# Kernel tuning notes

Hardware: AMD Instinct MI355X
Metric: run time of the kernel (lower is better)

## Reference

```python
import jax, jax.numpy as jnp
import numpy as np

DIM = 2048
N_HEADS = 16
HEAD_DIM = DIM // N_HEADS
GROUP_SIZE = 128
THRESHOLD = 0.5
EPS = 1e-8
B, T = 2, 2048


def _ternary_dequant(w):
    # groupwise absmean ternary quantize + dequant; DIM % GROUP_SIZE == 0 so no pad
    O, I = w.shape
    g = I // GROUP_SIZE
    wg = w.reshape(O, g, GROUP_SIZE)
    scale = jnp.clip(jnp.mean(jnp.abs(wg), axis=-1, keepdims=True), EPS)
    wn = wg / scale
    q = jnp.where(wn > THRESHOLD, 1.0, jnp.where(wn < -THRESHOLD, -1.0, 0.0))
    return (q * scale).reshape(O, I)


def _bitlinear(x, w):
    # STE: forward uses quantized weight
    w_ste = w + jax.lax.stop_gradient(_ternary_dequant(w) - w)
    return x @ w_ste.T


def _rope_tables(t, head_dim, base=10000.0):
    half = head_dim // 2
    inv_freq = 1.0 / (base ** (jnp.arange(half, dtype=jnp.float32) / half))
    freqs = jnp.outer(jnp.arange(t, dtype=jnp.float32), inv_freq)  # [T, half]
    return jnp.cos(freqs), jnp.sin(freqs)


def _apply_rope(x, cos, sin):
    # x: [B, H, T, D]
    d = x.shape[-1]
    x1, x2 = x[..., : d // 2], x[..., d // 2 :]
    cos = cos[None, None, :, :]
    sin = sin[None, None, :, :]
    return jnp.concatenate([x1 * cos - x2 * sin, x1 * sin + x2 * cos], axis=-1)


def setup_inputs() -> dict:
    key = jax.random.key(0)
    ks = jax.random.split(key, 5)
    std = 1.0 / np.sqrt(DIM)
    return {
        "x": jax.random.normal(ks[0], (B, T, DIM), dtype=jnp.float32),
        "w_q": jax.random.normal(ks[1], (DIM, DIM), dtype=jnp.float32) * std,
        "w_k": jax.random.normal(ks[2], (DIM, DIM), dtype=jnp.float32) * std,
        "w_v": jax.random.normal(ks[3], (DIM, DIM), dtype=jnp.float32) * std,
        "w_o": jax.random.normal(ks[4], (DIM, DIM), dtype=jnp.float32) * std,
    }


def reference(x, w_q, w_k, w_v, w_o):
    b, t, c = x.shape
    scale = HEAD_DIM ** -0.5

    def split_heads(y):
        return y.reshape(b, t, N_HEADS, HEAD_DIM).transpose(0, 2, 1, 3)  # [B,H,T,D]

    q = split_heads(_bitlinear(x, w_q))
    k = split_heads(_bitlinear(x, w_k))
    v = split_heads(_bitlinear(x, w_v))

    cos, sin = _rope_tables(t, HEAD_DIM)
    q = _apply_rope(q, cos, sin)
    k = _apply_rope(k, cos, sin)

    scores = jnp.einsum("bhqd,bhkd->bhqk", q, k) * scale
    causal = jnp.triu(jnp.ones((t, t), dtype=bool), k=1)
    scores = jnp.where(causal[None, None], -jnp.inf, scores)
    probs = jax.nn.softmax(scores, axis=-1)
    y = jnp.einsum("bhqk,bhkd->bhqd", probs, v)
    y = y.transpose(0, 2, 1, 3).reshape(b, t, c)
    return _bitlinear(y, w_o)
```

## Files before the change

### kernel.cpp

```cpp
#include <hip/hip_runtime.h>
#include <stdint.h>
#include <math.h>

#define DIMC 2048
#define NHEADS 16
#define HDIM 128
#define TSEQ 2048
#define NTOK 4096

using bf16x8 = __attribute__((ext_vector_type(8))) short;
using f32x4  = __attribute__((ext_vector_type(4))) float;

typedef __attribute__((address_space(1))) const void gas_void;
typedef __attribute__((address_space(3))) void las_void;

static __device__ __forceinline__ unsigned short f2b(float f) {
  union { float f; unsigned int u; } a; a.f = f;
  unsigned int u = a.u;
  u = (u + 0x7fffu + ((u >> 16) & 1u)) >> 16;
  return (unsigned short)u;
}
static __device__ __forceinline__ float b2f(unsigned short s) {
  union { unsigned int u; float f; } a; a.u = ((unsigned int)s) << 16;
  return a.f;
}

__global__ void detect_dtype(const unsigned short* __restrict__ xs,
                             int* __restrict__ flag)
{
  const int lane = threadIdx.x;
  const unsigned short u = xs[2 * lane];
  const int e = (u >> 7) & 0xFF;
  const bool plausible = (e >= 112) && (e <= 135);
  const unsigned long long m = __ballot(plausible);
  if (lane == 0) *flag = (__popcll(m) >= 32) ? 1 : 0;
}

static __device__ __forceinline__ void dequant_one(
    const void* __restrict__ w, unsigned short* __restrict__ o,
    int grp, int lane, int isbf16)
{
  float a, bq;
  if (isbf16) {
    const unsigned int pk =
        ((const unsigned int*)((const unsigned short*)w + (long)grp * 128))[lane];
    a  = b2f((unsigned short)(pk & 0xffffu));
    bq = b2f((unsigned short)(pk >> 16));
  } else {
    const float2 v = ((const float2*)((const float*)w + (long)grp * 128))[lane];
    a = v.x; bq = v.y;
  }
  double s = fabs((double)a) + fabs((double)bq);
  #pragma unroll
  for (int off = 1; off < 64; off <<= 1) s += __shfl_xor(s, off);
  double scale = s * (1.0 / 128.0);
  if (scale < 1e-8) scale = 1e-8;
  const float fs = (float)scale;
  const double wn0 = (double)a / scale;
  const double wn1 = (double)bq / scale;
  const float q0 = (wn0 > 0.5) ? fs : ((wn0 < -0.5) ? -fs : 0.0f);
  const float q1 = (wn1 > 0.5) ? fs : ((wn1 < -0.5) ? -fs : 0.0f);
  const unsigned int opk = (unsigned int)f2b(q0) | ((unsigned int)f2b(q1) << 16);
  ((unsigned int*)o)[(long)grp * 64 + lane] = opk;
}

__global__ void __launch_bounds__(256) dequant_auto(
    const void* __restrict__ w, unsigned short* __restrict__ o,
    const int* __restrict__ flag)
{
  const int wave = threadIdx.x >> 6, lane = threadIdx.x & 63;
  dequant_one(w, o, blockIdx.x * 4 + wave, lane, *flag);
}

__global__ void __launch_bounds__(256) dequant3(
    const void* __restrict__ w0, const void* __restrict__ w1,
    const void* __restrict__ w2, unsigned short* __restrict__ o,
    const int* __restrict__ flag)
{
  const int wave = threadIdx.x >> 6, lane = threadIdx.x & 63;
  const void* w = (blockIdx.y == 0) ? w0 : (blockIdx.y == 1) ? w1 : w2;
  unsigned short* oo = o + (long)blockIdx.y * DIMC * DIMC;
  dequant_one(w, oo, blockIdx.x * 4 + wave, lane, *flag);
}

__global__ void __launch_bounds__(256) cast_auto(
    const void* __restrict__ x, unsigned short* __restrict__ o,
    const int* __restrict__ flag)
{
  const int i = (blockIdx.x * 256 + threadIdx.x) * 4;
  if (*flag) {
    *(ushort4*)(o + i) = *(const ushort4*)((const unsigned short*)x + i);
  } else {
    const float4 v = *(const float4*)((const float*)x + i);
    ushort4 u;
    u.x = f2b(v.x); u.y = f2b(v.y); u.z = f2b(v.z); u.w = f2b(v.w);
    *(ushort4*)(o + i) = u;
  }
}

__device__ __forceinline__ void storeOne(float* C, long i, float v) { C[i] = v; }
__device__ __forceinline__ void storeOne(unsigned short* C, long i, float v) { C[i] = f2b(v); }

template <typename OUTT>
static __device__ __forceinline__ void gemm_tile(
    const unsigned short* __restrict__ A, const unsigned short* __restrict__ B,
    OUTT* __restrict__ C, int m0, int n0, int Nc, int K,
    unsigned short* As, unsigned short* Bs)
{
  const int tid = threadIdx.x;
  const int wave = tid >> 6;
  const int lane = tid & 63;
  const int wr = (wave >> 1) * 64, wc = (wave & 1) * 64;
  const int c16 = lane & 15, q4 = lane >> 4;

  f32x4 acc[4][4];
  #pragma unroll
  for (int i = 0; i < 4; i++)
    #pragma unroll
    for (int j = 0; j < 4; j++)
      acc[i][j] = (f32x4){0.f, 0.f, 0.f, 0.f};

  const int srow = tid >> 2;
  const int scol = (tid & 3) * 8;
  const unsigned short* ga = A + (long)(m0 + srow) * K + scol;
  const unsigned short* gb = B + (long)(n0 + srow) * K + scol;

  for (int k0 = 0; k0 < K; k0 += 64) {
    #pragma unroll
    for (int h = 0; h < 2; h++)
      #pragma unroll
      for (int i = 0; i < 2; i++) {
        __builtin_amdgcn_global_load_lds(
            (gas_void*)(ga + (long)i * 64 * K + k0 + h * 32),
            (las_void*)(As + h * 4096 + i * 2048 + wave * 512), 16, 0, 0);
        __builtin_amdgcn_global_load_lds(
            (gas_void*)(gb + (long)i * 64 * K + k0 + h * 32),
            (las_void*)(Bs + h * 4096 + i * 2048 + wave * 512), 16, 0, 0);
      }
    __syncthreads();
    #pragma unroll
    for (int kc = 0; kc < 2; kc++) {
      bf16x8 af[4], bfr[4];
      #pragma unroll
      for (int t = 0; t < 4; t++) {
        af[t]  = *(const bf16x8*)(As + kc * 4096 + (wr + t * 16 + c16) * 32 + q4 * 8);
        bfr[t] = *(const bf16x8*)(Bs + kc * 4096 + (wc + t * 16 + c16) * 32 + q4 * 8);
      }
      #pragma unroll
      for (int mt = 0; mt < 4; mt++)
        #pragma unroll
        for (int nt = 0; nt < 4; nt++)
          acc[mt][nt] = __builtin_amdgcn_mfma_f32_16x16x32_bf16(af[mt], bfr[nt], acc[mt][nt], 0, 0, 0);
    }
    __syncthreads();
  }

  #pragma unroll
  for (int mt = 0; mt < 4; mt++) {
    const int m = m0 + wr + mt * 16 + q4 * 4;
    #pragma unroll
    for (int nt = 0; nt < 4; nt++) {
      const int n = wc + nt * 16 + c16;
      #pragma unroll
      for (int r = 0; r < 4; r++)
        storeOne(C, (long)(m + r) * Nc + n, acc[mt][nt][r]);
    }
  }
}

template <typename OUTT>
__global__ void __launch_bounds__(256) gemm_bt(
    const unsigned short* __restrict__ A, const unsigned short* __restrict__ B,
    OUTT* __restrict__ C, int M, int N, int K)
{
  __shared__ unsigned short As[128 * 64];
  __shared__ unsigned short Bs[128 * 64];
  gemm_tile<OUTT>(A, B, C + blockIdx.x * 128, blockIdx.y * 128, blockIdx.x * 128,
                  N, K, As, Bs);
}

__global__ void __launch_bounds__(256) gemm_qkv(
    const unsigned short* __restrict__ A, const unsigned short* __restrict__ B,
    unsigned short* __restrict__ C0, unsigned short* __restrict__ C1,
    unsigned short* __restrict__ C2, int K)
{
  __shared__ unsigned short As[128 * 64];
  __shared__ unsigned short Bs[128 * 64];
  const int n0 = blockIdx.x * 128;
  unsigned short* Cb = (n0 < 2048) ? C0 : (n0 < 4096) ? C1 : C2;
  gemm_tile<unsigned short>(A, B, Cb + (n0 & 2047), blockIdx.y * 128, n0,
                            DIMC, K, As, Bs);
}

__global__ void __launch_bounds__(256) rope_kernel(
    unsigned short* __restrict__ Q, unsigned short* __restrict__ Kb)
{
  const int idx = blockIdx.x * 256 + threadIdx.x;
  const int d = idx & 63;
  const int h = (idx >> 6) & (NHEADS - 1);
  const int row = idx >> 10;
  const int t = row & (TSEQ - 1);
  const float inv_freq = expf(-9.210340371976184f * (float)d * (1.0f / 64.0f));
  float sn, cs;
  sincosf((float)t * inv_freq, &sn, &cs);
  const long base = (long)row * DIMC + h * HDIM + d;
  float x1 = b2f(Q[base]), x2 = b2f(Q[base + 64]);
  Q[base]      = f2b(x1 * cs - x2 * sn);
  Q[base + 64] = f2b(x1 * sn + x2 * cs);
  x1 = b2f(Kb[base]); x2 = b2f(Kb[base + 64]);
  Kb[base]      = f2b(x1 * cs - x2 * sn);
  Kb[base + 64] = f2b(x1 * sn + x2 * cs);
}

#define FA_M 16.0f
__global__ void __launch_bounds__(256) fattn(
    const unsigned short* __restrict__ Q,
    const unsigned short* __restrict__ K,
    const unsigned short* __restrict__ V,
    unsigned short* __restrict__ Y)
{
  __shared__ unsigned short SU[9216];
  __shared__ unsigned short VT[128 * 72];
  __shared__ float red[4][32];

  const int tid = threadIdx.x, wave = tid >> 6, lane = tid & 63;
  const int idx = blockIdx.x;
  const int qt = 15 - (idx >> 5);
  const int bh = idx & 31;
  const int b = bh >> 4, h = bh & 15;
  const int qbase = qt * 128;
  const int qw = wave * 32;
  const int c = lane & 15, g = lane >> 4;
  const long tokbase = (long)b * TSEQ;
  const int col0 = h * HDIM;

  bf16x8 qf[2][4];
  #pragma unroll
  for (int qq = 0; qq < 2; qq++) {
    const unsigned short* qp =
        Q + (tokbase + qbase + qw + qq * 16 + c) * DIMC + col0 + g * 8;
    #pragma unroll
    for (int kc = 0; kc < 4; kc++) qf[qq][kc] = *(const bf16x8*)(qp + kc * 32);
  }

  f32x4 od[8][2];
  #pragma unroll
  for (int dt = 0; dt < 8; dt++)
    #pragma unroll
    for (int qq = 0; qq < 2; qq++)
      od[dt][qq] = (f32x4){0.f, 0.f, 0.f, 0.f};
  float lpart[2][4];
  #pragma unroll
  for (int qq = 0; qq < 2; qq++)
    #pragma unroll
    for (int r = 0; r < 4; r++) lpart[qq][r] = 0.0f;

  const int ksr = tid >> 2, ksc = (tid & 3) * 32;
  const int vk0 = (tid & 31) * 2, vd0 = (tid >> 5) * 16;

  const float SC = 0.088388347648318447f;
  const int nkt = 2 * qt + 2;

  float4 kr0, kr1, kr2, kr3;
  bf16x8 va0, va1, vb0, vb1;
  {
    const unsigned short* src = K + (tokbase + ksr) * DIMC + col0 + ksc;
    kr0 = ((const float4*)src)[0]; kr1 = ((const float4*)src)[1];
    kr2 = ((const float4*)src)[2]; kr3 = ((const float4*)src)[3];
    const unsigned short* s0 = V + (tokbase + vk0) * DIMC + col0 + vd0;
    const unsigned short* s1 = s0 + DIMC;
    va0 = *(const bf16x8*)(s0); va1 = *(const bf16x8*)(s0 + 8);
    vb0 = *(const bf16x8*)(s1); vb1 = *(const bf16x8*)(s1 + 8);
  }

  for (int kt = 0; kt < nkt; kt++) {
    const int kb = kt * 64;
    __syncthreads();
    {
      float4* dst = (float4*)&SU[ksr * 136 + ksc];
      dst[0] = kr0; dst[1] = kr1; dst[2] = kr2; dst[3] = kr3;
    }
    {
      #pragma unroll
      for (int dd = 0; dd < 8; dd++) {
        const unsigned int p0 =
            (unsigned int)(unsigned short)va0[dd] |
            ((unsigned int)(unsigned short)vb0[dd] << 16);
        *(unsigned int*)&VT[(vd0 + dd) * 72 + vk0] = p0;
      }
      #pragma unroll
      for (int dd = 0; dd < 8; dd++) {
        const unsigned int p1 =
            (unsigned int)(unsigned short)va1[dd] |
            ((unsigned int)(unsigned short)vb1[dd] << 16);
        *(unsigned int*)&VT[(vd0 + 8 + dd) * 72 + vk0] = p1;
      }
    }
    __syncthreads();

    if (kt + 1 < nkt) {
      const int kb2 = kb + 64;
      const unsigned short* src = K + (tokbase + kb2 + ksr) * DIMC + col0 + ksc;
      kr0 = ((const float4*)src)[0]; kr1 = ((const float4*)src)[1];
      kr2 = ((const float4*)src)[2]; kr3 = ((const float4*)src)[3];
      const unsigned short* s0 = V + (tokbase + kb2 + vk0) * DIMC + col0 + vd0;
      const unsigned short* s1 = s0 + DIMC;
      va0 = *(const bf16x8*)(s0); va1 = *(const bf16x8*)(s0 + 8);
      vb0 = *(const bf16x8*)(s1); vb1 = *(const bf16x8*)(s1 + 8);
    }

    f32x4 sacc[2][4];
    #pragma unroll
    for (int qq = 0; qq < 2; qq++)
      #pragma unroll
      for (int nt = 0; nt < 4; nt++) sacc[qq][nt] = (f32x4){0.f, 0.f, 0.f, 0.f};
    #pragma unroll
    for (int kc = 0; kc < 4; kc++) {
      bf16x8 bk[4];
      #pragma unroll
      for (int nt = 0; nt < 4; nt++)
        bk[nt] = *(const bf16x8*)&SU[(nt * 16 + c) * 136 + kc * 32 + g * 8];
      #pragma unroll
      for (int qq = 0; qq < 2; qq++)
        #pragma unroll
        for (int nt = 0; nt < 4; nt++)
          sacc[qq][nt] = __builtin_amdgcn_mfma_f32_16x16x32_bf16(
              qf[qq][kc], bk[nt], sacc[qq][nt], 0, 0, 0);
    }
    __syncthreads();

    #pragma unroll
    for (int qq = 0; qq < 2; qq++)
      #pragma unroll
      for (int r = 0; r < 4; r++) {
        const int qg = qbase + qw + qq * 16 + g * 4 + r;
        #pragma unroll
        for (int nt = 0; nt < 4; nt++) {
          const int kg = kb + nt * 16 + c;
          const float sv = sacc[qq][nt][r] * SC - FA_M;
          const float p = (kg > qg) ? 0.0f : __expf(sv);
          lpart[qq][r] += p;
          SU[(wave * 32 + qq * 16 + g * 4 + r) * 72 + nt * 16 + c] = f2b(p);
        }
      }

    #pragma unroll
    for (int kc = 0; kc < 2; kc++) {
      bf16x8 pb[2];
      #pragma unroll
      for (int qq = 0; qq < 2; qq++)
        pb[qq] = *(const bf16x8*)&SU[(wave * 32 + qq * 16 + c) * 72 + kc * 32 + g * 8];
      #pragma unroll
      for (int dt = 0; dt < 8; dt++) {
        bf16x8 va = *(const bf16x8*)&VT[(dt * 16 + c) * 72 + kc * 32 + g * 8];
        #pragma unroll
        for (int qq = 0; qq < 2; qq++)
          od[dt][qq] = __builtin_amdgcn_mfma_f32_16x16x32_bf16(
              va, pb[qq], od[dt][qq], 0, 0, 0);
      }
    }
  }

  #pragma unroll
  for (int qq = 0; qq < 2; qq++)
    #pragma unroll
    for (int r = 0; r < 4; r++) {
      float l = lpart[qq][r];
      #pragma unroll
      for (int off = 1; off < 16; off <<= 1) l += __shfl_xor(l, off);
      lpart[qq][r] = l;
    }
  __syncthreads();
  if (c == 0) {
    #pragma unroll
    for (int qq = 0; qq < 2; qq++)
      #pragma unroll
      for (int r = 0; r < 4; r++)
        red[wave][qq * 16 + g * 4 + r] = 1.0f / lpart[qq][r];
  }
  __syncthreads();
  #pragma unroll
  for (int qq = 0; qq < 2; qq++) {
    const float linv = red[wave][qq * 16 + c];
    unsigned short* yp =
        Y + (tokbase + qbase + qw + qq * 16 + c) * DIMC + col0;
    #pragma unroll
    for (int dt = 0; dt < 8; dt++)
      #pragma unroll
      for (int r = 0; r < 4; r++)
        yp[dt * 16 + g * 4 + r] = f2b(od[dt][qq][r] * linv);
  }
}

extern "C" void kernel_launch(void* const* d_in, const int* in_sizes, int n_in,
                              void* d_out, int out_size, void* d_ws, size_t ws_size,
                              hipStream_t stream)
{
  const void* x  = d_in[0];
  const void* wq = d_in[1];
  const void* wk = d_in[2];
  const void* wv = d_in[3];
  const void* wo = d_in[4];
  float* out = (float*)d_out;

  char* ws = (char*)d_ws;
  const size_t MB = 1024 * 1024;
  unsigned short* wbuf = (unsigned short*)(ws + 0 * MB);
  unsigned short* xb   = (unsigned short*)(ws + 24 * MB);
  unsigned short* Qb   = (unsigned short*)(ws + 40 * MB);
  unsigned short* Kb   = (unsigned short*)(ws + 56 * MB);
  unsigned short* Vb   = (unsigned short*)(ws + 72 * MB);
  int* flag            = (int*)(ws + 88 * MB);
  unsigned short* Yb   = xb;

  detect_dtype<<<dim3(1), 64, 0, stream>>>((const unsigned short*)x, flag);
  cast_auto<<<dim3(8192), 256, 0, stream>>>(x, xb, flag);
  dequant3<<<dim3(8192, 3), 256, 0, stream>>>(wq, wk, wv, wbuf, flag);
  gemm_qkv<<<dim3(48, 32), 256, 0, stream>>>(xb, wbuf, Qb, Kb, Vb, DIMC);
  rope_kernel<<<dim3(16384), 256, 0, stream>>>(Qb, Kb);
  fattn<<<dim3(512), 256, 0, stream>>>(Qb, Kb, Vb, Yb);
  dequant_auto<<<dim3(8192), 256, 0, stream>>>(wo, wbuf, flag);
  gemm_bt<float><<<dim3(16, 32), 256, 0, stream>>>(Yb, wbuf, out, NTOK, DIMC, DIMC);
}
```

Before: 403.4 us.

## Replace QKV GEMM with 256x256 eight-wave pipelined MFMA kernel

Swaps the 128x128 single-buffered QKV projection GEMM for a 256x256 tile kernel with 8 waves. It double-buffers LDS, stages tiles with direct global-to-LDS loads and interleaves quarter-tile MFMA phases with the prefetch of the next K slice, raising s_setprio around the MFMA bursts. The aim is more operand reuse per block and hiding global-load latency behind compute. The cost is more barriers, higher register and LDS pressure, and only 384 blocks, which may leave some of the GPU's CUs underused.

```diff
diff --git a/kernel.cpp b/kernel.cpp
--- a/kernel.cpp
+++ b/kernel.cpp
@@ -179,17 +179,152 @@
                   N, K, As, Bs);
 }
 
-__global__ void __launch_bounds__(256) gemm_qkv(
-    const unsigned short* __restrict__ A, const unsigned short* __restrict__ B,
+__global__ void __launch_bounds__(512, 2) gemm8_qkv(
+    const unsigned short* __restrict__ A, const unsigned short* __restrict__ Bm,
     unsigned short* __restrict__ C0, unsigned short* __restrict__ C1,
     unsigned short* __restrict__ C2, int K)
 {
-  __shared__ unsigned short As[128 * 64];
-  __shared__ unsigned short Bs[128 * 64];
-  const int n0 = blockIdx.x * 128;
+  __shared__ unsigned short sm[2][2][2][8192];
+
+  const int tid = threadIdx.x;
+  const int w = tid >> 6, lane = tid & 63;
+  const int wr = w >> 2, wc = w & 3;
+  const int wh = wc >> 1, wb = (wc & 1) * 4;
+  const int c16 = lane & 15, q4 = lane >> 4;
+  const int swz = (c16 * 32 + q4 * 8) ^ ((c16 & 8) ? 16 : 0);
+  const int srow = lane >> 2;
+  const int scol = ((lane & 3) * 8) ^ ((lane & 32) ? 16 : 0);
+  const int rg0 = w >> 1, cg = w & 1;
+
+  const int n0 = blockIdx.x * 256, m0 = blockIdx.y * 256;
+  const int NT = K >> 6;
+
+  f32x4 acc[8][4];
+  #pragma unroll
+  for (int i = 0; i < 8; i++)
+    #pragma unroll
+    for (int j = 0; j < 4; j++) acc[i][j] = (f32x4){0.f, 0.f, 0.f, 0.f};
+
+  auto stage = [&](const unsigned short* __restrict__ G, int rowbase, int kt,
+                   unsigned short* dst) {
+    #pragma unroll
+    for (int l = 0; l < 2; l++) {
+      const unsigned short* s = G +
+          (long)(rowbase + (rg0 + l * 4) * 16 + srow) * K + kt * 64 + cg * 32 + scol;
+      __builtin_amdgcn_global_load_lds((gas_void*)s,
+          (las_void*)(dst + (l * 8 + w) * 512), 16, 0, 0);
+    }
+  };
+
+  stage(A,  m0,       0, &sm[0][0][0][0]);
+  stage(A,  m0 + 128, 0, &sm[0][0][1][0]);
+  stage(Bm, n0,       0, &sm[0][1][0][0]);
+  stage(Bm, n0 + 128, 0, &sm[0][1][1][0]);
+  stage(Bm, n0,       1, &sm[1][1][0][0]);
+  stage(Bm, n0 + 128, 1, &sm[1][1][1][0]);
+  asm volatile("s_waitcnt vmcnt(4)" ::: "memory");
+  __builtin_amdgcn_s_barrier();
+
+  bf16x8 af[4][2], b01[2][2], b23[2][2];
+
+  for (int t = 0; t < NT; ++t) {
+    const int cur = t & 1, nxt = cur ^ 1;
+
+    #pragma unroll
+    for (int m = 0; m < 4; m++)
+      #pragma unroll
+      for (int kk = 0; kk < 2; kk++)
+        af[m][kk] = *(const bf16x8*)&sm[cur][0][wr][m * 1024 + kk * 512 + swz];
+    #pragma unroll
+    for (int n = 0; n < 2; n++)
+      #pragma unroll
+      for (int kk = 0; kk < 2; kk++)
+        b01[n][kk] = *(const bf16x8*)&sm[cur][1][wh][(wb + n) * 1024 + kk * 512 + swz];
+    if (t + 1 < NT) stage(A, m0, t + 1, &sm[nxt][0][0][0]);
+    __builtin_amdgcn_s_barrier();
+    asm volatile("s_waitcnt lgkmcnt(0)" ::: "memory");
+    __builtin_amdgcn_s_setprio(1);
+    #pragma unroll
+    for (int kk = 0; kk < 2; kk++)
+      #pragma unroll
+      for (int m = 0; m < 4; m++)
+        #pragma unroll
+        for (int n = 0; n < 2; n++)
+          acc[m][n] = __builtin_amdgcn_mfma_f32_16x16x32_bf16(
+              af[m][kk], b01[n][kk], acc[m][n], 0, 0, 0);
+    __builtin_amdgcn_s_setprio(0);
+    __builtin_amdgcn_s_barrier();
+
+    #pragma unroll
+    for (int n = 0; n < 2; n++)
+      #pragma unroll
+      for (int kk = 0; kk < 2; kk++)
+        b23[n][kk] = *(const bf16x8*)&sm[cur][1][wh][(wb + 2 + n) * 1024 + kk * 512 + swz];
+    if (t + 1 < NT) stage(A, m0 + 128, t + 1, &sm[nxt][0][1][0]);
+    __builtin_amdgcn_s_barrier();
+    asm volatile("s_waitcnt lgkmcnt(0)" ::: "memory");
+    __builtin_amdgcn_s_setprio(1);
+    #pragma unroll
+    for (int kk = 0; kk < 2; kk++)
+      #pragma unroll
+      for (int m = 0; m < 4; m++)
+        #pragma unroll
+        for (int n = 0; n < 2; n++)
+          acc[m][2 + n] = __builtin_amdgcn_mfma_f32_16x16x32_bf16(
+              af[m][kk], b23[n][kk], acc[m][2 + n], 0, 0, 0);
+    __builtin_amdgcn_s_setprio(0);
+    __builtin_amdgcn_s_barrier();
+
+    #pragma unroll
+    for (int m = 0; m < 4; m++)
+      #pragma unroll
+      for (int kk = 0; kk < 2; kk++)
+        af[m][kk] = *(const bf16x8*)&sm[cur][0][wr][(4 + m) * 1024 + kk * 512 + swz];
+    if (t + 2 < NT) stage(Bm, n0, t + 2, &sm[cur][1][0][0]);
+    __builtin_amdgcn_s_barrier();
+    asm volatile("s_waitcnt lgkmcnt(0)" ::: "memory");
+    __builtin_amdgcn_s_setprio(1);
+    #pragma unroll
+    for (int kk = 0; kk < 2; kk++)
+      #pragma unroll
+      for (int m = 0; m < 4; m++)
+        #pragma unroll
+        for (int n = 0; n < 2; n++)
+          acc[4 + m][2 + n] = __builtin_amdgcn_mfma_f32_16x16x32_bf16(
+              af[m][kk], b23[n][kk], acc[4 + m][2 + n], 0, 0, 0);
+    __builtin_amdgcn_s_setprio(0);
+    __builtin_amdgcn_s_barrier();
+
+    if (t + 2 < NT) stage(Bm, n0 + 128, t + 2, &sm[cur][1][1][0]);
+    __builtin_amdgcn_s_barrier();
+    __builtin_amdgcn_s_setprio(1);
+    #pragma unroll
+    for (int kk = 0; kk < 2; kk++)
+      #pragma unroll
+      for (int m = 0; m < 4; m++)
+        #pragma unroll
+        for (int n = 0; n < 2; n++)
+          acc[4 + m][n] = __builtin_amdgcn_mfma_f32_16x16x32_bf16(
+              af[m][kk], b01[n][kk], acc[4 + m][n], 0, 0, 0);
+    __builtin_amdgcn_s_setprio(0);
+    if (t + 2 < NT) { asm volatile("s_waitcnt vmcnt(4)" ::: "memory"); }
+    else            { asm volatile("s_waitcnt vmcnt(0)" ::: "memory"); }
+    __builtin_amdgcn_s_barrier();
+  }
+
   unsigned short* Cb = (n0 < 2048) ? C0 : (n0 < 4096) ? C1 : C2;
-  gemm_tile<unsigned short>(A, B, Cb + (n0 & 2047), blockIdx.y * 128, n0,
-                            DIMC, K, As, Bs);
+  const int nloc = (n0 & 2047) + wc * 64;
+  #pragma unroll
+  for (int mt = 0; mt < 8; mt++) {
+    const int m = m0 + wr * 128 + mt * 16 + q4 * 4;
+    #pragma unroll
+    for (int nt = 0; nt < 4; nt++) {
+      const int n = nloc + nt * 16 + c16;
+      #pragma unroll
+      for (int r = 0; r < 4; r++)
+        Cb[(long)(m + r) * DIMC + n] = f2b(acc[mt][nt][r]);
+    }
+  }
 }
 
 __global__ void __launch_bounds__(256) rope_kernel(
@@ -416,7 +551,7 @@
   detect_dtype<<<dim3(1), 64, 0, stream>>>((const unsigned short*)x, flag);
   cast_auto<<<dim3(8192), 256, 0, stream>>>(x, xb, flag);
   dequant3<<<dim3(8192, 3), 256, 0, stream>>>(wq, wk, wv, wbuf, flag);
-  gemm_qkv<<<dim3(48, 32), 256, 0, stream>>>(xb, wbuf, Qb, Kb, Vb, DIMC);
+  gemm8_qkv<<<dim3(24, 16), 512, 0, stream>>>(xb, wbuf, Qb, Kb, Vb, DIMC);
   rope_kernel<<<dim3(16384), 256, 0, stream>>>(Qb, Kb);
   fattn<<<dim3(512), 256, 0, stream>>>(Qb, Kb, Vb, Yb);
   dequant_auto<<<dim3(8192), 256, 0, stream>>>(wo, wbuf, flag);
```

New measurement: 408.6 us. Within noise of the previous version (+1.3%).

## Fuse dtype detection, casting and all weight dequants; swizzle attention LDS layout

Applied to the files above, without the earlier changes.

Merges the dtype detection, input cast and the QKV and output weight dequantisation into one prep kernel. Each wave now detects the dtype inline instead of reading a flag written by a separate launch. When the workspace is large enough, the output weight is dequantised up front into its own buffer, which removes two launches. In the attention kernel, the padded LDS rows (136/72 strides) are replaced with unpadded rows and an XOR swizzle, which aims to avoid bank conflicts while shrinking shared memory use. The risks are the extra ballot work in every wave and a dependence on the size of the workspace.

```diff
diff --git a/kernel.cpp b/kernel.cpp
--- a/kernel.cpp
+++ b/kernel.cpp
@@ -25,15 +25,13 @@
   return a.f;
 }
 
-__global__ void detect_dtype(const unsigned short* __restrict__ xs,
-                             int* __restrict__ flag)
-{
-  const int lane = threadIdx.x;
-  const unsigned short u = xs[2 * lane];
+static __device__ __forceinline__ int detect_inline(const void* __restrict__ x)
+{
+  const int lane = threadIdx.x & 63;
+  const unsigned short u = ((const unsigned short*)x)[2 * lane];
   const int e = (u >> 7) & 0xFF;
-  const bool plausible = (e >= 112) && (e <= 135);
-  const unsigned long long m = __ballot(plausible);
-  if (lane == 0) *flag = (__popcll(m) >= 32) ? 1 : 0;
+  const unsigned long long m = __ballot((e >= 112) && (e <= 135));
+  return (__popcll(m) >= 32) ? 1 : 0;
 }
 
 static __device__ __forceinline__ void dequant_one(
@@ -64,38 +62,42 @@
   ((unsigned int*)o)[(long)grp * 64 + lane] = opk;
 }
 
+__global__ void __launch_bounds__(256) prep(
+    const void* __restrict__ x,
+    const void* __restrict__ w0, const void* __restrict__ w1,
+    const void* __restrict__ w2, const void* __restrict__ w3,
+    unsigned short* __restrict__ xb, unsigned short* __restrict__ wqkv,
+    unsigned short* __restrict__ wob)
+{
+  const int isbf16 = detect_inline(x);
+  const int wave = threadIdx.x >> 6, lane = threadIdx.x & 63;
+  const int y = blockIdx.y;
+  if (y == 0) {
+    const int i = (blockIdx.x * 256 + threadIdx.x) * 4;
+    if (isbf16) {
+      *(ushort4*)(xb + i) = *(const ushort4*)((const unsigned short*)x + i);
+    } else {
+      const float4 v = *(const float4*)((const float*)x + i);
+      ushort4 u;
+      u.x = f2b(v.x); u.y = f2b(v.y); u.z = f2b(v.z); u.w = f2b(v.w);
+      *(ushort4*)(xb + i) = u;
+    }
+  } else if (y <= 3) {
+    const void* w = (y == 1) ? w0 : (y == 2) ? w1 : w2;
+    dequant_one(w, wqkv + (long)(y - 1) * DIMC * DIMC,
+                blockIdx.x * 4 + wave, lane, isbf16);
+  } else {
+    dequant_one(w3, wob, blockIdx.x * 4 + wave, lane, isbf16);
+  }
+}
+
 __global__ void __launch_bounds__(256) dequant_auto(
-    const void* __restrict__ w, unsigned short* __restrict__ o,
-    const int* __restrict__ flag)
-{
-  const int wave = threadIdx.x >> 6, lane = threadIdx.x & 63;
-  dequant_one(w, o, blockIdx.x * 4 + wave, lane, *flag);
-}
-
-__global__ void __launch_bounds__(256) dequant3(
-    const void* __restrict__ w0, const void* __restrict__ w1,
-    const void* __restrict__ w2, unsigned short* __restrict__ o,
-    const int* __restrict__ flag)
-{
-  const int wave = threadIdx.x >> 6, lane = threadIdx.x & 63;
-  const void* w = (blockIdx.y == 0) ? w0 : (blockIdx.y == 1) ? w1 : w2;
-  unsigned short* oo = o + (long)blockIdx.y * DIMC * DIMC;
-  dequant_one(w, oo, blockIdx.x * 4 + wave, lane, *flag);
-}
-
-__global__ void __launch_bounds__(256) cast_auto(
-    const void* __restrict__ x, unsigned short* __restrict__ o,
-    const int* __restrict__ flag)
-{
-  const int i = (blockIdx.x * 256 + threadIdx.x) * 4;
-  if (*flag) {
-    *(ushort4*)(o + i) = *(const ushort4*)((const unsigned short*)x + i);
-  } else {
-    const float4 v = *(const float4*)((const float*)x + i);
-    ushort4 u;
-    u.x = f2b(v.x); u.y = f2b(v.y); u.z = f2b(v.z); u.w = f2b(v.w);
-    *(ushort4*)(o + i) = u;
-  }
+    const void* __restrict__ w, const void* __restrict__ x,
+    unsigned short* __restrict__ o)
+{
+  const int isbf16 = detect_inline(x);
+  dequant_one(w, o, blockIdx.x * 4 + (threadIdx.x >> 6), threadIdx.x & 63,
+              isbf16);
 }
 
 __device__ __forceinline__ void storeOne(float* C, long i, float v) { C[i] = v; }
@@ -212,6 +214,9 @@
   Kb[base + 64] = f2b(x1 * sn + x2 * cs);
 }
 
+static __device__ __forceinline__ int swz(int row, int idx) {
+  return idx ^ ((row & 7) << 3);
+}
 #define FA_M 16.0f
 __global__ void __launch_bounds__(256) fattn(
     const unsigned short* __restrict__ Q,
@@ -219,8 +224,8 @@
     const unsigned short* __restrict__ V,
     unsigned short* __restrict__ Y)
 {
-  __shared__ unsigned short SU[9216];
-  __shared__ unsigned short VT[128 * 72];
+  __shared__ unsigned short SU[8192];
+  __shared__ unsigned short VT[8192];
   __shared__ float red[4][32];
 
   const int tid = threadIdx.x, wave = tid >> 6, lane = tid & 63;
@@ -277,8 +282,11 @@
     const int kb = kt * 64;
     __syncthreads();
     {
-      float4* dst = (float4*)&SU[ksr * 136 + ksc];
-      dst[0] = kr0; dst[1] = kr1; dst[2] = kr2; dst[3] = kr3;
+      unsigned short* krow = &SU[ksr * 128];
+      *(float4*)&krow[swz(ksr, ksc + 0)]  = kr0;
+      *(float4*)&krow[swz(ksr, ksc + 8)]  = kr1;
+      *(float4*)&krow[swz(ksr, ksc + 16)] = kr2;
+      *(float4*)&krow[swz(ksr, ksc + 24)] = kr3;
     }
     {
       #pragma unroll
@@ -286,14 +294,14 @@
         const unsigned int p0 =
             (unsigned int)(unsigned short)va0[dd] |
             ((unsigned int)(unsigned short)vb0[dd] << 16);
-        *(unsigned int*)&VT[(vd0 + dd) * 72 + vk0] = p0;
+        *(unsigned int*)&VT[(vd0 + dd) * 64 + swz(vd0 + dd, vk0)] = p0;
       }
       #pragma unroll
       for (int dd = 0; dd < 8; dd++) {
         const unsigned int p1 =
             (unsigned int)(unsigned short)va1[dd] |
             ((unsigned int)(unsigned short)vb1[dd] << 16);
-        *(unsigned int*)&VT[(vd0 + 8 + dd) * 72 + vk0] = p1;
+        *(unsigned int*)&VT[(vd0 + 8 + dd) * 64 + swz(vd0 + 8 + dd, vk0)] = p1;
       }
     }
     __syncthreads();
@@ -318,8 +326,10 @@
     for (int kc = 0; kc < 4; kc++) {
       bf16x8 bk[4];
       #pragma unroll
-      for (int nt = 0; nt < 4; nt++)
-        bk[nt] = *(const bf16x8*)&SU[(nt * 16 + c) * 136 + kc * 32 + g * 8];
+      for (int nt = 0; nt < 4; nt++) {
+        const int kr = nt * 16 + c;
+        bk[nt] = *(const bf16x8*)&SU[kr * 128 + swz(kr, kc * 32 + g * 8)];
+      }
       #pragma unroll
       for (int qq = 0; qq < 2; qq++)
         #pragma unroll
@@ -334,13 +344,14 @@
       #pragma unroll
       for (int r = 0; r < 4; r++) {
         const int qg = qbase + qw + qq * 16 + g * 4 + r;
+        const int prow = qw + qq * 16 + g * 4 + r;
         #pragma unroll
         for (int nt = 0; nt < 4; nt++) {
           const int kg = kb + nt * 16 + c;
           const float sv = sacc[qq][nt][r] * SC - FA_M;
           const float p = (kg > qg) ? 0.0f : __expf(sv);
           lpart[qq][r] += p;
-          SU[(wave * 32 + qq * 16 + g * 4 + r) * 72 + nt * 16 + c] = f2b(p);
+          SU[prow * 64 + swz(prow, nt * 16 + c)] = f2b(p);
         }
       }
 
@@ -348,11 +359,14 @@
     for (int kc = 0; kc < 2; kc++) {
       bf16x8 pb[2];
       #pragma unroll
-      for (int qq = 0; qq < 2; qq++)
-        pb[qq] = *(const bf16x8*)&SU[(wave * 32 + qq * 16 + c) * 72 + kc * 32 + g * 8];
+      for (int qq = 0; qq < 2; qq++) {
+        const int prow = qw + qq * 16 + c;
+        pb[qq] = *(const bf16x8*)&SU[prow * 64 + swz(prow, kc * 32 + g * 8)];
+      }
       #pragma unroll
       for (int dt = 0; dt < 8; dt++) {
-        bf16x8 va = *(const bf16x8*)&VT[(dt * 16 + c) * 72 + kc * 32 + g * 8];
+        const int vr = dt * 16 + c;
+        bf16x8 va = *(const bf16x8*)&VT[vr * 64 + swz(vr, kc * 32 + g * 8)];
         #pragma unroll
         for (int qq = 0; qq < 2; qq++)
           od[dt][qq] = __builtin_amdgcn_mfma_f32_16x16x32_bf16(
@@ -410,15 +424,22 @@
   unsigned short* Qb   = (unsigned short*)(ws + 40 * MB);
   unsigned short* Kb   = (unsigned short*)(ws + 56 * MB);
   unsigned short* Vb   = (unsigned short*)(ws + 72 * MB);
-  int* flag            = (int*)(ws + 88 * MB);
+  unsigned short* wob  = (unsigned short*)(ws + 88 * MB);
   unsigned short* Yb   = xb;
 
-  detect_dtype<<<dim3(1), 64, 0, stream>>>((const unsigned short*)x, flag);
-  cast_auto<<<dim3(8192), 256, 0, stream>>>(x, xb, flag);
-  dequant3<<<dim3(8192, 3), 256, 0, stream>>>(wq, wk, wv, wbuf, flag);
+  const int wo_in_prep = (ws_size >= 97 * MB) ? 1 : 0;
+
+  prep<<<dim3(8192, wo_in_prep ? 5 : 4), 256, 0, stream>>>(
+      x, wq, wk, wv, wo, xb, wbuf, wob);
   gemm_qkv<<<dim3(48, 32), 256, 0, stream>>>(xb, wbuf, Qb, Kb, Vb, DIMC);
   rope_kernel<<<dim3(16384), 256, 0, stream>>>(Qb, Kb);
   fattn<<<dim3(512), 256, 0, stream>>>(Qb, Kb, Vb, Yb);
-  dequant_auto<<<dim3(8192), 256, 0, stream>>>(wo, wbuf, flag);
-  gemm_bt<float><<<dim3(16, 32), 256, 0, stream>>>(Yb, wbuf, out, NTOK, DIMC, DIMC);
-}
+  const unsigned short* wo_b;
+  if (wo_in_prep) {
+    wo_b = wob;
+  } else {
+    dequant_auto<<<dim3(8192), 256, 0, stream>>>(wo, x, wbuf);
+    wo_b = wbuf;
+  }
+  gemm_bt<float><<<dim3(16, 32), 256, 0, stream>>>(Yb, wo_b, out, NTOK, DIMC, DIMC);
+}
```

Measured after the change: 413.7 us. +2.5%, slower.
